# Optimization experiments

Hardware: AMD Instinct MI355X
Metric: run time of the kernel (lower is better)

Reference implementation:

```python
import jax, jax.numpy as jnp
import numpy as np
import math

# irreps: 512x0 + 512x1 + 512x2 + 512x3 + 512x4 (SO3), mul_ir layout
LS = [0, 1, 2, 3, 4]
MULS = [512, 512, 512, 512, 512]
LMAX = 4
N = 4096
DIM = sum(m * (2 * l + 1) for m, l in zip(MULS, LS))  # 12800


def _small_d(l, beta):
    """Complex Wigner small-d matrix d^l_{m',m}(beta), m ordered -l..l (numpy, static)."""
    d = np.zeros((2 * l + 1, 2 * l + 1))
    cb, sb = math.cos(beta / 2.0), math.sin(beta / 2.0)
    for i, mp in enumerate(range(-l, l + 1)):
        for j, m in enumerate(range(-l, l + 1)):
            num = math.sqrt(math.factorial(l + mp) * math.factorial(l - mp)
                            * math.factorial(l + m) * math.factorial(l - m))
            tot = 0.0
            for s in range(max(0, m - mp), min(l + m, l - mp) + 1):
                den = (math.factorial(l + m - s) * math.factorial(s)
                       * math.factorial(mp - m + s) * math.factorial(l - mp - s))
                tot += ((-1.0) ** (mp - m + s)) * num / den \
                       * cb ** (2 * l + m - mp - 2 * s) * sb ** (mp - m + 2 * s)
            d[i, j] = tot
    return d


def _real_basis(l):
    """Unitary complex->real spherical-harmonic change of basis A (rows: real m=-l..l)."""
    A = np.zeros((2 * l + 1, 2 * l + 1), dtype=complex)
    A[l, l] = 1.0
    inv_s2 = 1.0 / math.sqrt(2.0)
    for m in range(1, l + 1):
        A[l + m, l + m] = ((-1) ** m) * inv_s2
        A[l + m, l - m] = inv_s2
        A[l - m, l + m] = -1j * ((-1) ** m) * inv_s2
        A[l - m, l - m] = 1j * inv_s2
    return A


def _J(l):
    """Real Wigner-D of the +pi/2 rotation that maps the 'easy' axis onto x.
    Conjugating the closed-form easy-axis rotation by J gives the x-axis rotation."""
    A = _real_basis(l)
    Dc = _small_d(l, math.pi / 2.0).astype(complex)
    return np.real(A @ Dc @ A.conj().T).astype(np.float32)


_JS = {l: _J(l) for l in LS if l > 0}


def _encode(angle, lmax):
    """[cos(l a), ..., cos(a), 1, sin(a), ..., sin(l a)] exactly as encode_rotation_angle."""
    m = jnp.arange(1, lmax + 1, dtype=angle.dtype)
    a = angle[:, None]
    c = jnp.cos(m * a)
    s = jnp.sin(m * a)
    return jnp.concatenate([c[:, ::-1], jnp.ones_like(a), s], axis=-1)  # [N, 2*lmax+1]


def _easy(enc, l, lmax):
    """Per-sample easy-axis rotation matrix for degree l built from the angle encoding.
    Rows/cols ordered m = -l..l: diag cos(|m|a), antidiag -sin(m a)."""
    d = 2 * l + 1
    m = np.arange(-l, l + 1)
    sign = np.sign(m).astype(np.float32)
    cos_v = enc[:, lmax - np.abs(m)]                 # [N, d] cos(|m| a)
    sin_v = enc[:, lmax + np.abs(m)] * sign          # [N, d] sin(m a)
    i = np.arange(d)
    E = jnp.zeros((enc.shape[0], d, d), enc.dtype)
    E = E.at[:, i, i].set(cos_v)
    E = E.at[:, i, d - 1 - i].add(-sin_v)            # add: center (m=0) overlaps diag, sin(0)=0
    return E


def _rotate(gamma, beta, alpha, x):
    n = x.shape[0]
    eg = _encode(gamma, LMAX)
    eb = _encode(beta, LMAX)
    ea = _encode(alpha, LMAX)
    outs = []
    off = 0
    for mul, l in zip(MULS, LS):
        d = 2 * l + 1
        seg = x[:, off:off + mul * d].reshape(n, mul, d)
        off += mul * d
        if l == 0:
            outs.append(seg.reshape(n, mul))  # scalars are rotation-invariant
            continue
        J = jnp.asarray(_JS[l], dtype=x.dtype)
        Eg = _easy(eg, l, LMAX)
        Eb = _easy(eb, l, LMAX)
        Ea = _easy(ea, l, LMAX)
        # yxy rotation: D = E(alpha) . J . E(beta) . J^T . E(gamma)
        D = Ea @ jnp.matmul(J, Eb @ jnp.matmul(J.T, Eg))  # [N, d, d]
        outs.append(jnp.einsum('nij,nuj->nui', D, seg).reshape(n, mul * d))
    return jnp.concatenate(outs, axis=-1)


def setup_inputs() -> dict:
    key = jax.random.key(0)
    kg, kb, ka, kx = jax.random.split(key, 4)
    pi = math.pi
    return {
        'gamma': jax.random.uniform(kg, (N,), jnp.float32, -pi, pi),
        'beta': jax.random.uniform(kb, (N,), jnp.float32, -pi, pi),
        'alpha': jax.random.uniform(ka, (N,), jnp.float32, -pi, pi),
        'x': jax.random.normal(kx, (N, DIM), jnp.float32),
    }


def reference(gamma, beta, alpha, x):
    return _rotate(gamma, beta, alpha, x)
```

## Files before the change

kernel.cpp:

```cpp
#include <hip/hip_runtime.h>
#include <math.h>

#define NSAMP 4096
#define DIMX  12800

#define JTOT 164

__global__ __launch_bounds__(256) void initJ_kernel(float* __restrict__ Jout) {
    __shared__ double dm[JTOT];
    __shared__ double Ar[JTOT], Ai[JTOT];
    __shared__ double Br[JTOT], Bi[JTOT];

    const int tid = threadIdx.x;
    int l = 0, base = 0, d = 0, ii = 0, jj = 0;
    const bool act = tid < JTOT;
    if (act) {
        if (tid < 9)       { l = 1; base = 0; }
        else if (tid < 34) { l = 2; base = 9; }
        else if (tid < 83) { l = 3; base = 34; }
        else               { l = 4; base = 83; }
        d = 2 * l + 1;
        int loc = tid - base;
        ii = loc / d;
        jj = loc - ii * d;

        double fact[9];
        fact[0] = 1.0;
        for (int k = 1; k < 9; k++) fact[k] = fact[k - 1] * (double)k;

        const int mp = ii - l, m = jj - l;
        const double num = sqrt(fact[l + mp] * fact[l - mp] * fact[l + m] * fact[l - m]);
        const double c2 = 0.70710678118654752440;
        double tot = 0.0;
        const int s0 = (m - mp > 0) ? (m - mp) : 0;
        const int s1 = (l + m < l - mp) ? (l + m) : (l - mp);
        for (int s = s0; s <= s1; s++) {
            double den = fact[l + m - s] * fact[s] * fact[mp - m + s] * fact[l - mp - s];
            int etot = (2 * l + m - mp - 2 * s) + (mp - m + 2 * s);
            double p = 1.0;
            for (int q = 0; q < etot; q++) p *= c2;
            double sgn = ((mp - m + s) & 1) ? -1.0 : 1.0;
            tot += sgn * (num / den) * p;
        }
        dm[tid] = tot;

        double ar = 0.0, ai = 0.0;
        const double inv_s2 = 0.70710678118654752440;
        if (ii == l) {
            if (jj == l) ar = 1.0;
        } else if (ii > l) {
            int mm = ii - l;
            if (jj == l + mm)      ar = (mm & 1) ? -inv_s2 : inv_s2;
            else if (jj == l - mm) ar = inv_s2;
        } else {
            int mm = l - ii;
            if (jj == l + mm)      ai = (mm & 1) ? inv_s2 : -inv_s2;
            else if (jj == l - mm) ai = inv_s2;
        }
        Ar[tid] = ar; Ai[tid] = ai;
    }
    __syncthreads();
    if (act) {
        double br = 0.0, bi = 0.0;
        for (int k = 0; k < d; k++) {
            double dv = dm[base + k * d + jj];
            br += Ar[base + ii * d + k] * dv;
            bi += Ai[base + ii * d + k] * dv;
        }
        Br[tid] = br; Bi[tid] = bi;
    }
    __syncthreads();
    if (act) {
        double jr = 0.0;
        for (int k = 0; k < d; k++) {
            jr += Br[base + ii * d + k] * Ar[base + jj * d + k]
                + Bi[base + ii * d + k] * Ai[base + jj * d + k];
        }
        Jout[tid] = (float)jr;
    }
}

template <int L>
__device__ __forceinline__ void apply_l(const float* __restrict__ xs_base,
                                        float* __restrict__ os_base,
                                        const float* __restrict__ Dl, int tid) {
    constexpr int d = 2 * L + 1;
#pragma unroll
    for (int rep = 0; rep < 2; rep++) {
        const int g = tid + rep * 256;
        const float* xs = xs_base + g * d;
        float v[d];
#pragma unroll
        for (int j = 0; j < d; j++) v[j] = xs[j];
        float r[d];
#pragma unroll
        for (int i = 0; i < d; i++) {
            float acc = 0.0f;
#pragma unroll
            for (int j = 0; j < d; j++) acc = fmaf(Dl[i * d + j], v[j], acc);
            r[i] = acc;
        }
        float* os = os_base + g * d;
#pragma unroll
        for (int i = 0; i < d; i++) os[i] = r[i];
    }
}

__global__ __launch_bounds__(256) void rot_main(
    const float* __restrict__ gamma, const float* __restrict__ beta,
    const float* __restrict__ alpha, const float* __restrict__ x,
    const float* __restrict__ Jws, float* __restrict__ out) {
    __shared__ float sJ[JTOT];
    __shared__ float sD[JTOT];
    __shared__ float sT0[JTOT];
    __shared__ float sT1[JTOT];
    __shared__ float trig[3][10];

    const int tid = threadIdx.x;
    const int n = blockIdx.x;

    if (tid < JTOT) sJ[tid] = Jws[tid];
    if (tid < 30) {
        int ai = tid / 10, k = tid % 10;
        float ang = (ai == 0) ? gamma[n] : (ai == 1) ? beta[n] : alpha[n];
        trig[ai][k] = (k < 5) ? cosf((float)k * ang) : sinf((float)(k - 5) * ang);
    }
    __syncthreads();

    int l = 0, base = 0, d = 0, ii = 0, jj = 0;
    const bool act = tid < JTOT;
    if (act) {
        if (tid < 9)       { l = 1; base = 0; }
        else if (tid < 34) { l = 2; base = 9; }
        else if (tid < 83) { l = 3; base = 34; }
        else               { l = 4; base = 83; }
        d = 2 * l + 1;
        int loc = tid - base;
        ii = loc / d;
        jj = loc - ii * d;
    }
    if (act) {
        int am = jj - l, aa = (am < 0) ? -am : am;
        float cv = trig[0][aa];
        float sv = (am > 0) ? trig[0][5 + aa] : (am < 0) ? -trig[0][5 + aa] : 0.0f;
        sT0[tid] = sJ[base + jj * d + ii] * cv + sJ[base + (d - 1 - jj) * d + ii] * sv;
    }
    __syncthreads();
    if (act) {
        int am = ii - l, aa = (am < 0) ? -am : am;
        float cv = trig[1][aa];
        float sv = (am > 0) ? trig[1][5 + aa] : (am < 0) ? -trig[1][5 + aa] : 0.0f;
        sT1[tid] = cv * sT0[tid] - sv * sT0[base + (d - 1 - ii) * d + jj];
    }
    __syncthreads();
    if (act) {
        float acc = 0.0f;
        for (int k = 0; k < d; k++)
            acc = fmaf(sJ[base + ii * d + k], sT1[base + k * d + jj], acc);
        sT0[tid] = acc;
    }
    __syncthreads();
    if (act) {
        int am = ii - l, aa = (am < 0) ? -am : am;
        float cv = trig[2][aa];
        float sv = (am > 0) ? trig[2][5 + aa] : (am < 0) ? -trig[2][5 + aa] : 0.0f;
        sD[tid] = cv * sT0[tid] - sv * sT0[base + (d - 1 - ii) * d + jj];
    }
    __syncthreads();

    const float* xrow = x + (size_t)n * DIMX;
    float* orow = out + (size_t)n * DIMX;

    {
        const float2* xv = (const float2*)xrow;
        float2* ov = (float2*)orow;
        ov[tid] = xv[tid];
    }
    apply_l<1>(xrow + 512,  orow + 512,  &sD[0],  tid);
    apply_l<2>(xrow + 2048, orow + 2048, &sD[9],  tid);
    apply_l<3>(xrow + 4608, orow + 4608, &sD[34], tid);
    apply_l<4>(xrow + 8192, orow + 8192, &sD[83], tid);
}

extern "C" void kernel_launch(void* const* d_in, const int* in_sizes, int n_in,
                              void* d_out, int out_size, void* d_ws, size_t ws_size,
                              hipStream_t stream) {
    const float* gamma = (const float*)d_in[0];
    const float* beta  = (const float*)d_in[1];
    const float* alpha = (const float*)d_in[2];
    const float* x     = (const float*)d_in[3];
    float* out = (float*)d_out;
    float* Jws = (float*)d_ws;

    hipLaunchKernelGGL(initJ_kernel, dim3(1), dim3(256), 0, stream, Jws);
    hipLaunchKernelGGL(rot_main, dim3(NSAMP), dim3(256), 0, stream,
                       gamma, beta, alpha, x, Jws, out);
}
```

Before: 362.7 us.

## Stage per-irrep segments through LDS for coalesced float4 loads and stores

Each irrep segment is now loaded into a shared-memory buffer with coalesced float4 accesses, rotated in place in LDS, and written back to global memory with coalesced float4 stores. Before, each thread read and wrote d strided floats directly from global memory. The l=1 segment load is also issued before the Wigner-D construction so it overlaps the matrix setup. The cost is an 18 KB LDS buffer, which may limit occupancy, plus extra barriers and possible LDS bank conflicts from the stride-d accesses.

```diff
diff --git a/kernel.cpp b/kernel.cpp
--- a/kernel.cpp
+++ b/kernel.cpp
@@ -80,18 +80,31 @@
     }
 }
 
-template <int L>
-__device__ __forceinline__ void apply_l(const float* __restrict__ xs_base,
-                                        float* __restrict__ os_base,
-                                        const float* __restrict__ Dl, int tid) {
-    constexpr int d = 2 * L + 1;
+template <int L, bool STAGE_IN>
+__device__ __forceinline__ void seg_l(const float* __restrict__ xs,
+                                      float* __restrict__ os,
+                                      const float* __restrict__ Dl,
+                                      float* __restrict__ buf, int tid) {
+    constexpr int d   = 2 * L + 1;
+    constexpr int nf4 = 512 * d / 4;
+    constexpr int full = nf4 / 256;
+    constexpr int rem  = nf4 - full * 256;
+
+    float4* bv = (float4*)buf;
+    if (STAGE_IN) {
+        const float4* xv = (const float4*)xs;
+#pragma unroll
+        for (int q = 0; q < full; q++) bv[tid + q * 256] = xv[tid + q * 256];
+        if (tid < rem) bv[tid + full * 256] = xv[tid + full * 256];
+        __syncthreads();
+    }
+
 #pragma unroll
     for (int rep = 0; rep < 2; rep++) {
         const int g = tid + rep * 256;
-        const float* xs = xs_base + g * d;
         float v[d];
 #pragma unroll
-        for (int j = 0; j < d; j++) v[j] = xs[j];
+        for (int j = 0; j < d; j++) v[j] = buf[g * d + j];
         float r[d];
 #pragma unroll
         for (int i = 0; i < d; i++) {
@@ -100,10 +113,16 @@
             for (int j = 0; j < d; j++) acc = fmaf(Dl[i * d + j], v[j], acc);
             r[i] = acc;
         }
-        float* os = os_base + g * d;
-#pragma unroll
-        for (int i = 0; i < d; i++) os[i] = r[i];
-    }
+#pragma unroll
+        for (int i = 0; i < d; i++) buf[g * d + i] = r[i];
+    }
+    __syncthreads();
+
+    float4* ov = (float4*)os;
+#pragma unroll
+    for (int q = 0; q < full; q++) ov[tid + q * 256] = bv[tid + q * 256];
+    if (tid < rem) ov[tid + full * 256] = bv[tid + full * 256];
+    __syncthreads();
 }
 
 __global__ __launch_bounds__(256) void rot_main(
@@ -115,15 +134,28 @@
     __shared__ float sT0[JTOT];
     __shared__ float sT1[JTOT];
     __shared__ float trig[3][10];
+    __shared__ __align__(16) float xbuf[4608];
 
     const int tid = threadIdx.x;
     const int n = blockIdx.x;
+
+    const float* xrow = x + (size_t)n * DIMX;
+    float* orow = out + (size_t)n * DIMX;
 
     if (tid < JTOT) sJ[tid] = Jws[tid];
     if (tid < 30) {
         int ai = tid / 10, k = tid % 10;
         float ang = (ai == 0) ? gamma[n] : (ai == 1) ? beta[n] : alpha[n];
         trig[ai][k] = (k < 5) ? cosf((float)k * ang) : sinf((float)(k - 5) * ang);
+    }
+    {
+        const float4* xv = (const float4*)(xrow + 512);
+        float4* bv = (float4*)xbuf;
+        bv[tid] = xv[tid];
+        if (tid < 128) bv[tid + 256] = xv[tid + 256];
+        const float2* x2 = (const float2*)xrow;
+        float2* o2 = (float2*)orow;
+        o2[tid] = x2[tid];
     }
     __syncthreads();
 
@@ -168,18 +200,10 @@
     }
     __syncthreads();
 
-    const float* xrow = x + (size_t)n * DIMX;
-    float* orow = out + (size_t)n * DIMX;
-
-    {
-        const float2* xv = (const float2*)xrow;
-        float2* ov = (float2*)orow;
-        ov[tid] = xv[tid];
-    }
-    apply_l<1>(xrow + 512,  orow + 512,  &sD[0],  tid);
-    apply_l<2>(xrow + 2048, orow + 2048, &sD[9],  tid);
-    apply_l<3>(xrow + 4608, orow + 4608, &sD[34], tid);
-    apply_l<4>(xrow + 8192, orow + 8192, &sD[83], tid);
+    seg_l<1, false>(xrow + 512,  orow + 512,  &sD[0],  xbuf, tid);
+    seg_l<2, true >(xrow + 2048, orow + 2048, &sD[9],  xbuf, tid);
+    seg_l<3, true >(xrow + 4608, orow + 4608, &sD[34], xbuf, tid);
+    seg_l<4, true >(xrow + 8192, orow + 8192, &sD[83], xbuf, tid);
 }
 
 extern "C" void kernel_launch(void* const* d_in, const int* in_sizes, int n_in,
```

New measurement: 363.6 us. Within noise of the previous version (+0.3%).

## Stage x rows in LDS via async global_load_lds, overlapped with D-matrix setup

Applied to the files above, without the earlier changes.

Each block now issues 16-byte global_load_lds DMA transfers that copy its whole row of l>0 features into a 48KB LDS buffer before it computes the Wigner-D matrices, so the load overlaps that setup work. The per-l transforms then run in place in LDS. The row is written back with fully coalesced float4 stores, replacing the earlier strided per-thread global reads and writes of d-element groups. The cost is much higher LDS use per block (launch bounds ask for 3 blocks per CU), which limits occupancy. It also relies on the compiler waiting for the async LDS loads to finish before the barrier.

```diff
diff --git a/kernel.cpp b/kernel.cpp
--- a/kernel.cpp
+++ b/kernel.cpp
@@ -80,18 +80,23 @@
     }
 }
 
-template <int L>
-__device__ __forceinline__ void apply_l(const float* __restrict__ xs_base,
-                                        float* __restrict__ os_base,
-                                        const float* __restrict__ Dl, int tid) {
+__device__ __forceinline__ void gload_lds16(const float4* g, float* lds) {
+    __builtin_amdgcn_global_load_lds(
+        (const __attribute__((address_space(1))) void*)g,
+        (__attribute__((address_space(3))) void*)lds, 16, 0, 0);
+}
+
+template <int L, int SEGBASE>
+__device__ __forceinline__ void xform(float* __restrict__ buf,
+                                      const float* __restrict__ Dl, int tid) {
     constexpr int d = 2 * L + 1;
 #pragma unroll
     for (int rep = 0; rep < 2; rep++) {
         const int g = tid + rep * 256;
-        const float* xs = xs_base + g * d;
+        float* p = buf + SEGBASE + g * d;
         float v[d];
 #pragma unroll
-        for (int j = 0; j < d; j++) v[j] = xs[j];
+        for (int j = 0; j < d; j++) v[j] = p[j];
         float r[d];
 #pragma unroll
         for (int i = 0; i < d; i++) {
@@ -100,13 +105,12 @@
             for (int j = 0; j < d; j++) acc = fmaf(Dl[i * d + j], v[j], acc);
             r[i] = acc;
         }
-        float* os = os_base + g * d;
-#pragma unroll
-        for (int i = 0; i < d; i++) os[i] = r[i];
-    }
-}
-
-__global__ __launch_bounds__(256) void rot_main(
+#pragma unroll
+        for (int i = 0; i < d; i++) p[i] = r[i];
+    }
+}
+
+__global__ __launch_bounds__(256, 3) void rot_main(
     const float* __restrict__ gamma, const float* __restrict__ beta,
     const float* __restrict__ alpha, const float* __restrict__ x,
     const float* __restrict__ Jws, float* __restrict__ out) {
@@ -115,9 +119,25 @@
     __shared__ float sT0[JTOT];
     __shared__ float sT1[JTOT];
     __shared__ float trig[3][10];
+    __shared__ __align__(16) float xbuf[12288];
 
     const int tid = threadIdx.x;
     const int n = blockIdx.x;
+
+    const float* xrow = x + (size_t)n * DIMX;
+    float* orow = out + (size_t)n * DIMX;
+
+    const float2 l0 = ((const float2*)xrow)[tid];
+
+    {
+        const float4* xv4 = (const float4*)(xrow + 512);
+        float* ldsw = xbuf + ((tid >> 6) << 8);
+#pragma unroll
+        for (int q = 0; q < 12; q++)
+            gload_lds16(xv4 + q * 256 + tid, ldsw + q * 1024);
+    }
+
+    ((float2*)orow)[tid] = l0;
 
     if (tid < JTOT) sJ[tid] = Jws[tid];
     if (tid < 30) {
@@ -168,18 +188,19 @@
     }
     __syncthreads();
 
-    const float* xrow = x + (size_t)n * DIMX;
-    float* orow = out + (size_t)n * DIMX;
+    xform<1, 0>(xbuf, &sD[0], tid);
+    xform<2, 1536>(xbuf, &sD[9], tid);
+    xform<3, 4096>(xbuf, &sD[34], tid);
+    xform<4, 7680>(xbuf, &sD[83], tid);
+    __syncthreads();
 
     {
-        const float2* xv = (const float2*)xrow;
-        float2* ov = (float2*)orow;
-        ov[tid] = xv[tid];
-    }
-    apply_l<1>(xrow + 512,  orow + 512,  &sD[0],  tid);
-    apply_l<2>(xrow + 2048, orow + 2048, &sD[9],  tid);
-    apply_l<3>(xrow + 4608, orow + 4608, &sD[34], tid);
-    apply_l<4>(xrow + 8192, orow + 8192, &sD[83], tid);
+        float4* ov4 = (float4*)(orow + 512);
+        const float4* bv4 = (const float4*)xbuf;
+#pragma unroll
+        for (int q = 0; q < 12; q++)
+            ov4[q * 256 + tid] = bv4[q * 256 + tid];
+    }
 }
 
 extern "C" void kernel_launch(void* const* d_in, const int* in_sizes, int n_in,
```

Result: no change. 365.0 us (+0.6%).
